# Kernel optimization log

Measured on AMD Instinct MI355X. Metric: run time of the kernel, lower is better.

Reference implementation:

```python
import math
import jax, jax.numpy as jnp
import numpy as np

B, S, H = 4, 2048, 1024      # batch, seq_len, hidden_size
E, K, I = 8, 2, 1024         # n_routed_experts, top_k, expert intermediate
NSH = 2                      # n_shared_experts -> shared intermediate = NSH*I
CF, RSF = 1.25, 1.0          # capacity_factor, routed_scaling_factor


def setup_inputs() -> dict:
    key = jax.random.key(0)
    ks = jax.random.split(key, 8)
    w = lambda k, sh: jax.random.normal(k, sh, dtype=jnp.float32) * 0.02
    return {
        "hidden_states": jax.random.normal(ks[0], (B, S, H), dtype=jnp.float32),
        "gate_w":  w(ks[1], (E, H)),          # router weight (torch Linear layout)
        "we_gate": w(ks[2], (E, I, H)),       # per-expert gate_proj
        "we_up":   w(ks[3], (E, I, H)),       # per-expert up_proj
        "we_down": w(ks[4], (E, H, I)),       # per-expert down_proj
        "ws_gate": w(ks[5], (NSH * I, H)),    # shared expert gate_proj
        "ws_up":   w(ks[6], (NSH * I, H)),
        "ws_down": w(ks[7], (H, NSH * I)),
    }


def reference(hidden_states, gate_w, we_gate, we_up, we_down, ws_gate, ws_up, ws_down):
    orig_shape = hidden_states.shape
    x = hidden_states.reshape(-1, H)                       # [N, H]
    N = x.shape[0]

    # ---- gate (fp32 softmax + top-k, normalized, scaled) ----
    logits = x.astype(jnp.float32) @ gate_w.astype(jnp.float32).T   # [N, E]
    scores = jax.nn.softmax(logits, axis=-1)
    topk_w, topk_idx = jax.lax.top_k(scores, K)                      # [N, K]
    topk_w = topk_w / (topk_w.sum(-1, keepdims=True) + 1e-20) * RSF  # norm_topk_prob

    # ---- capacity masking: position of each (token,k) slot within its expert ----
    capacity = math.ceil(CF * N * K / E)
    flat = topk_idx.reshape(-1)                                      # [N*K]
    one_hot = jax.nn.one_hot(flat, E, dtype=jnp.int32)               # [N*K, E]
    pos = jnp.cumsum(one_hot, axis=0) - 1                            # running count per expert
    pos_tok = jnp.take_along_axis(pos, flat[:, None], axis=1)[:, 0]  # [N*K]
    keep = (pos_tok < capacity).reshape(N, K)
    topk_w = topk_w * keep.astype(topk_w.dtype)

    # ---- combine weights per (token, expert); dropped slots contribute 0 ----
    comb = jnp.zeros((N, E), jnp.float32).at[jnp.arange(N)[:, None], topk_idx].add(topk_w)

    # ---- routed experts: dense SwiGLU per expert, weighted combine ----
    g = jnp.einsum('nh,eih->nei', x, we_gate)                        # [N, E, I]
    u = jnp.einsum('nh,eih->nei', x, we_up)
    eo = jnp.einsum('nei,ehi->neh', jax.nn.silu(g) * u, we_down)     # [N, E, H]
    y = jnp.einsum('neh,ne->nh', eo, comb)                           # [N, H]

    # ---- shared experts ----
    sh = (jax.nn.silu(x @ ws_gate.T) * (x @ ws_up.T)) @ ws_down.T    # [N, H]

    return (y + sh).reshape(orig_shape)
```

## Files before the change

kernel.cpp:

```cpp
#include <hip/hip_runtime.h>

typedef unsigned short u16;

#define NTOK 8192
#define HD   1024
#define NEXP 8
#define CAP  2560

typedef __bf16 bf16x8 __attribute__((ext_vector_type(8)));
typedef float  f32x4  __attribute__((ext_vector_type(4)));

__device__ __forceinline__ u16 f2bf(float f){
  union { float f; unsigned u; } v; v.f = f;
  return (u16)((v.u + 0x7fffu + ((v.u >> 16) & 1u)) >> 16);
}
__device__ __forceinline__ float bf2f(u16 h){
  union { unsigned u; float f; } v; v.u = ((unsigned)h) << 16; return v.f;
}

__device__ __forceinline__ void async16(const void* g, void* l){
  __builtin_amdgcn_global_load_lds((__attribute__((address_space(1))) void*)(g),
                                   (__attribute__((address_space(3))) void*)(l), 16, 0, 0);
}

__global__ __launch_bounds__(256)
void prep_kernel(const float* __restrict__ x, const float* __restrict__ gate_w,
                 const float* __restrict__ we_gate, const float* __restrict__ we_up,
                 const float* __restrict__ we_down, const float* __restrict__ ws_gate,
                 const float* __restrict__ ws_up, const float* __restrict__ ws_down,
                 u16* __restrict__ x_bf, u16* __restrict__ wg_bf, u16* __restrict__ wu_bf,
                 u16* __restrict__ wd_bf, u16* __restrict__ wsg_bf, u16* __restrict__ wsu_bf,
                 u16* __restrict__ wsd_bf,
                 int* __restrict__ topk_idx, float* __restrict__ topk_w){
  __shared__ float gw[NEXP * HD];
  int bid = blockIdx.x;
  int t = threadIdx.x;
  if (bid < 2048){
    for (int i = t; i < NEXP * HD; i += 256) gw[i] = gate_w[i];
    __syncthreads();
    int wave = t >> 6, l = t & 63;
    int tok = bid * 4 + wave;
    const float* xr = x + (size_t)tok * HD;
    double acc[NEXP];
#pragma unroll
    for (int e = 0; e < NEXP; e++) acc[e] = 0.0;
    for (int j = 0; j < 16; j++){
      int h = j * 64 + l;
      double xv = (double)xr[h];
#pragma unroll
      for (int e = 0; e < NEXP; e++) acc[e] += xv * (double)gw[e * HD + h];
    }
#pragma unroll
    for (int e = 0; e < NEXP; e++){
      double v = acc[e];
#pragma unroll
      for (int off = 32; off > 0; off >>= 1) v += __shfl_down(v, off, 64);
      acc[e] = v;
    }
    if (l == 0){
      int i0 = 0; double l0 = acc[0];
#pragma unroll
      for (int e = 1; e < NEXP; e++) if (acc[e] > l0){ l0 = acc[e]; i0 = e; }
      int i1 = -1; double l1 = -1e300;
#pragma unroll
      for (int e = 0; e < NEXP; e++) if (e != i0 && acc[e] > l1){ l1 = acc[e]; i1 = e; }
      double e1 = exp(l1 - l0);
      double s  = 1.0 + e1;
      topk_idx[tok * 2 + 0] = i0;
      topk_idx[tok * 2 + 1] = i1;
      topk_w [tok * 2 + 0] = (float)(1.0 / s);
      topk_w [tok * 2 + 1] = (float)(e1 / s);
    }
  } else {
    long long g = (long long)(bid - 2048) * 256 + t;
    const float4* s; ushort4* d; long long off;
    if      (g <  2097152){ s = (const float4*)x;       d = (ushort4*)x_bf;   off = 0; }
    else if (g <  4194304){ s = (const float4*)we_gate; d = (ushort4*)wg_bf;  off = 2097152; }
    else if (g <  6291456){ s = (const float4*)we_up;   d = (ushort4*)wu_bf;  off = 4194304; }
    else if (g <  8388608){ s = (const float4*)we_down; d = (ushort4*)wd_bf;  off = 6291456; }
    else if (g <  8912896){ s = (const float4*)ws_gate; d = (ushort4*)wsg_bf; off = 8388608; }
    else if (g <  9437184){ s = (const float4*)ws_up;   d = (ushort4*)wsu_bf; off = 8912896; }
    else                  { s = (const float4*)ws_down; d = (ushort4*)wsd_bf; off = 9437184; }
    long long i = g - off;
    float4 v = s[i];
    ushort4 o;
    o.x = f2bf(v.x); o.y = f2bf(v.y); o.z = f2bf(v.z); o.w = f2bf(v.w);
    d[i] = o;
  }
}

__global__ __launch_bounds__(256) void scan_kernel(const int* __restrict__ topk_idx,
                                                   const float* __restrict__ topk_w,
                                                   int* __restrict__ tok_list,
                                                   float* __restrict__ w_list,
                                                   int* __restrict__ slot_map,
                                                   int* __restrict__ ne){
  __shared__ int hist[256][NEXP];
  int t = threadIdx.x;
  const int SPT = (NTOK * 2) / 256;
  int cnt[NEXP];
#pragma unroll
  for (int e = 0; e < NEXP; e++) cnt[e] = 0;
  int base = t * SPT;
  for (int s = 0; s < SPT; s++) cnt[topk_idx[base + s]]++;
#pragma unroll
  for (int e = 0; e < NEXP; e++) hist[t][e] = cnt[e];
  __syncthreads();
  if (t < NEXP){
    int run = 0;
    for (int i = 0; i < 256; i++){ int v = hist[i][t]; hist[i][t] = run; run += v; }
    ne[t] = run < CAP ? run : CAP;
  }
  __syncthreads();
  int pos[NEXP];
#pragma unroll
  for (int e = 0; e < NEXP; e++) pos[e] = hist[t][e];
  for (int s = 0; s < SPT; s++){
    int slot = base + s;
    int e = topk_idx[slot];
    int p = pos[e]++;
    if (p < CAP){
      tok_list[e * CAP + p] = slot >> 1;
      w_list [e * CAP + p] = topk_w[slot];
      slot_map[slot] = e * CAP + p;
    } else {
      slot_map[slot] = -1;
    }
  }
}

__global__ __launch_bounds__(256)
void gu_kernel(const u16* __restrict__ x_bf,
               const u16* __restrict__ wg, const u16* __restrict__ wu,
               const u16* __restrict__ wsg, const u16* __restrict__ wsu,
               u16* __restrict__ Hr, u16* __restrict__ Hs,
               const int* __restrict__ tok_list, const int* __restrict__ ne)
{
  __shared__ u16 As[128 * 64];
  __shared__ u16 Bs[128 * 64];

  const int bid = blockIdx.x;
  const bool routed = bid < 2560;
  int m0, n0, ldc, n_valid;
  const u16 *B0, *B1;
  u16* C;
  const int* tl = nullptr;
  if (routed){
    int e = bid / 320, r = bid % 320;
    m0 = (r / 16) * 128; n0 = (r % 16) * 64;
    B0 = wg + (size_t)e * (1024 * 1024);
    B1 = wu + (size_t)e * (1024 * 1024);
    C  = Hr + (size_t)e * (CAP * 1024);
    ldc = 1024;
    n_valid = ne[e];
    tl = tok_list + e * CAP;
    if (m0 >= n_valid) return;
  } else {
    int b2 = bid - 2560;
    n0 = (b2 / 64) * 64; m0 = (b2 % 64) * 128;
    B0 = wsg; B1 = wsu; C = Hs; ldc = 2048; n_valid = 1 << 30;
  }

  const int tid = threadIdx.x;
  const int wv  = tid >> 6;
  const int l   = tid & 63;
  const int lr  = l >> 3;
  const int cb  = (l & 7) ^ lr;

  const u16* aptr[4];
  const u16* bptr[4];
#pragma unroll
  for (int i = 0; i < 4; i++){
    int chunk = i * 4 + wv;
    int arow  = m0 + chunk * 8 + lr;
    if (routed){
      int r2 = arow < n_valid ? arow : (n_valid - 1);
      aptr[i] = x_bf + (size_t)tl[r2] * 1024 + cb * 8;
    } else {
      aptr[i] = x_bf + (size_t)arow * 1024 + cb * 8;
    }
    int rn = chunk * 8 + lr;
    int w  = rn >> 6;
    int jq = (rn >> 4) & 3;
    int rl = rn & 15;
    int icol = n0 + w * 32 + (jq & 1) * 16 + rl;
    bptr[i] = ((jq < 2) ? B0 : B1) + (size_t)icol * 1024 + cb * 8;
  }

  const int wm = wv & 1, wn = wv >> 1;
  const int col = l & 15, quad = l >> 4;
  const int rr = col & 7, ch = col >> 3;

  f32x4 acc[4][4];
#pragma unroll
  for (int i = 0; i < 4; i++)
#pragma unroll
    for (int j = 0; j < 4; j++)
      acc[i][j] = (f32x4){0.f, 0.f, 0.f, 0.f};

  for (int k0 = 0; k0 < 1024; k0 += 64){
#pragma unroll
    for (int i = 0; i < 4; i++){
      int chunk = i * 4 + wv;
      async16(aptr[i] + k0, &As[chunk * 512 + l * 8]);
      async16(bptr[i] + k0, &Bs[chunk * 512 + l * 8]);
    }
    __syncthreads();
#pragma unroll
    for (int s = 0; s < 2; s++){
      const int so = (rr * 8 + ((quad + s * 4) ^ rr)) * 8;
      bf16x8 a[4], b[4];
#pragma unroll
      for (int i = 0; i < 4; i++) a[i] = *(const bf16x8*)&As[(wm * 8 + i * 2 + ch) * 512 + so];
#pragma unroll
      for (int j = 0; j < 4; j++) b[j] = *(const bf16x8*)&Bs[(wn * 8 + j * 2 + ch) * 512 + so];
#pragma unroll
      for (int i = 0; i < 4; i++)
#pragma unroll
        for (int j = 0; j < 4; j++)
          acc[i][j] = __builtin_amdgcn_mfma_f32_16x16x32_bf16(a[i], b[j], acc[i][j], 0, 0, 0);
    }
    __syncthreads();
  }

#pragma unroll
  for (int i = 0; i < 4; i++)
#pragma unroll
    for (int r = 0; r < 4; r++){
      int row = m0 + wm * 64 + i * 16 + quad * 4 + r;
#pragma unroll
      for (int j = 0; j < 2; j++){
        int cg = n0 + wn * 32 + j * 16 + col;
        float g = acc[i][j][r], u = acc[i][j + 2][r];
        float h = (g / (1.f + __expf(-g))) * u;
        C[(size_t)row * ldc + cg] = f2bf(h);
      }
    }
}

#define MODE_WBF   1
#define MODE_FINAL 2

template<int MODE>
__global__ __launch_bounds__(256)
void gemm_bt(const u16* __restrict__ A, long long sAe,
             const u16* __restrict__ B0, long long sBe,
             void* __restrict__ Cv, long long sCe, int ldc,
             const float* __restrict__ w_list, const int* __restrict__ ne,
             const u16* __restrict__ Ebuf, const int* __restrict__ slot_map,
             int M, int K)
{
  __shared__ u16 As[128 * 64];
  __shared__ u16 Bs[128 * 64];

  const int e  = blockIdx.z;
  const int m0 = blockIdx.y * 128;
  const int n0 = blockIdx.x * 128;

  int n_valid = (MODE == MODE_WBF) ? ne[e] : M;
  if (m0 >= n_valid) return;

  const u16* Ae = A + (size_t)e * sAe;

  const int tid = threadIdx.x;
  const int wv  = tid >> 6;
  const int l   = tid & 63;
  const int lr  = l >> 3;
  const int cb  = (l & 7) ^ lr;

  const u16* aptr[4];
  const u16* bptr[4];
#pragma unroll
  for (int i = 0; i < 4; i++){
    int chunk = i * 4 + wv;
    int arow  = m0 + chunk * 8 + lr;
    aptr[i] = Ae + (size_t)arow * K + cb * 8;
    int brow = n0 + chunk * 8 + lr;
    bptr[i] = B0 + (size_t)e * sBe + (size_t)brow * K + cb * 8;
  }

  const int wm = wv & 1, wn = wv >> 1;
  const int col = l & 15, quad = l >> 4;
  const int rr = col & 7, ch = col >> 3;

  f32x4 acc[4][4];
#pragma unroll
  for (int i = 0; i < 4; i++)
#pragma unroll
    for (int j = 0; j < 4; j++)
      acc[i][j] = (f32x4){0.f, 0.f, 0.f, 0.f};

  for (int k0 = 0; k0 < K; k0 += 64){
#pragma unroll
    for (int i = 0; i < 4; i++){
      int chunk = i * 4 + wv;
      async16(aptr[i] + k0, &As[chunk * 512 + l * 8]);
      async16(bptr[i] + k0, &Bs[chunk * 512 + l * 8]);
    }
    __syncthreads();
#pragma unroll
    for (int s = 0; s < 2; s++){
      const int so = (rr * 8 + ((quad + s * 4) ^ rr)) * 8;
      bf16x8 a[4], b[4];
#pragma unroll
      for (int i = 0; i < 4; i++) a[i] = *(const bf16x8*)&As[(wm * 8 + i * 2 + ch) * 512 + so];
#pragma unroll
      for (int j = 0; j < 4; j++) b[j] = *(const bf16x8*)&Bs[(wn * 8 + j * 2 + ch) * 512 + so];
#pragma unroll
      for (int i = 0; i < 4; i++)
#pragma unroll
        for (int j = 0; j < 4; j++)
          acc[i][j] = __builtin_amdgcn_mfma_f32_16x16x32_bf16(a[i], b[j], acc[i][j], 0, 0, 0);
    }
    __syncthreads();
  }

  if (MODE == MODE_WBF){
    u16* C = (u16*)Cv + (size_t)e * sCe;
    const float* wl = w_list + e * CAP;
#pragma unroll
    for (int i = 0; i < 4; i++)
#pragma unroll
      for (int r = 0; r < 4; r++){
        int row = m0 + wm * 64 + i * 16 + quad * 4 + r;
        if (row < n_valid){
          float wgt = wl[row];
#pragma unroll
          for (int j = 0; j < 4; j++){
            int cg = n0 + wn * 64 + j * 16 + col;
            C[(size_t)row * ldc + cg] = f2bf(wgt * acc[i][j][r]);
          }
        }
      }
  } else {
    float* C = (float*)Cv;
#pragma unroll
    for (int i = 0; i < 4; i++)
#pragma unroll
      for (int r = 0; r < 4; r++){
        int row = m0 + wm * 64 + i * 16 + quad * 4 + r;
        int s0 = slot_map[row * 2 + 0];
        int s1 = slot_map[row * 2 + 1];
#pragma unroll
        for (int j = 0; j < 4; j++){
          int cg = n0 + wn * 64 + j * 16 + col;
          float v = acc[i][j][r];
          if (s0 >= 0) v += bf2f(Ebuf[(size_t)s0 * HD + cg]);
          if (s1 >= 0) v += bf2f(Ebuf[(size_t)s1 * HD + cg]);
          C[(size_t)row * HD + cg] = v;
        }
      }
  }
}

extern "C" void kernel_launch(void* const* d_in, const int* in_sizes, int n_in,
                              void* d_out, int out_size, void* d_ws, size_t ws_size,
                              hipStream_t stream){
  const float* x       = (const float*)d_in[0];
  const float* gate_w  = (const float*)d_in[1];
  const float* we_gate = (const float*)d_in[2];
  const float* we_up   = (const float*)d_in[3];
  const float* we_down = (const float*)d_in[4];
  const float* ws_gate = (const float*)d_in[5];
  const float* ws_up   = (const float*)d_in[6];
  const float* ws_down = (const float*)d_in[7];
  float* out = (float*)d_out;

  char* p = (char*)d_ws;
  u16* x_bf   = (u16*)p; p += (size_t)NTOK * HD * 2;
  u16* wg_bf  = (u16*)p; p += (size_t)NEXP * 1024 * 1024 * 2;
  u16* wu_bf  = (u16*)p; p += (size_t)NEXP * 1024 * 1024 * 2;
  u16* wsg_bf = (u16*)p; p += (size_t)2048 * 1024 * 2;
  u16* wsu_bf = (u16*)p; p += (size_t)2048 * 1024 * 2;
  u16* wd_bf  = (u16*)p; p += (size_t)NEXP * 1024 * 1024 * 2;
  u16* wsd_bf = (u16*)p; p += (size_t)1024 * 2048 * 2;
  u16* Hr     = (u16*)p; p += (size_t)NEXP * CAP * 1024 * 2;
  u16* Hs     = (u16*)p; p += (size_t)NTOK * 2048 * 2;
  int*   topk_idx = (int*)p;   p += (size_t)NTOK * 2 * 4;
  float* topk_w   = (float*)p; p += (size_t)NTOK * 2 * 4;
  int*   tok_list = (int*)p;   p += (size_t)NEXP * CAP * 4;
  float* w_list   = (float*)p; p += (size_t)NEXP * CAP * 4;
  int*   slot_map = (int*)p;   p += (size_t)NTOK * 2 * 4;
  int*   ne       = (int*)p;   p += 128;
  u16* Ebuf = wg_bf;

  prep_kernel<<<dim3(40960), dim3(256), 0, stream>>>(
      x, gate_w, we_gate, we_up, we_down, ws_gate, ws_up, ws_down,
      x_bf, wg_bf, wu_bf, wd_bf, wsg_bf, wsu_bf, wsd_bf, topk_idx, topk_w);

  scan_kernel<<<dim3(1), dim3(256), 0, stream>>>(topk_idx, topk_w, tok_list, w_list, slot_map, ne);

  gu_kernel<<<dim3(4608), dim3(256), 0, stream>>>(
      x_bf, wg_bf, wu_bf, wsg_bf, wsu_bf, Hr, Hs, tok_list, ne);

  const long long WEXP = 1024LL * 1024;
  const long long SLOT = (long long)CAP * 1024;

  gemm_bt<MODE_WBF><<<dim3(8, 20, 8), 256, 0, stream>>>(
      Hr, SLOT, wd_bf, WEXP, Ebuf, SLOT, 1024,
      w_list, ne, nullptr, nullptr, CAP, 1024);

  gemm_bt<MODE_FINAL><<<dim3(8, 64, 1), 256, 0, stream>>>(
      Hs, 0, wsd_bf, 0, out, 0, 1024,
      w_list, ne, Ebuf, slot_map, NTOK, 2048);
}
```

Before: 555.7 us.

## Parallelize routing scan, merge down GEMMs into one launch, split combine

The single-block scan becomes a two-pass multi-block scan that uses wave ballots and popcounts to assign capacity positions. The routed and shared down-projection GEMMs now run in one launch, so their blocks can occupy the device together. The gather-add of routed outputs moves into a separate vectorized combine kernel. Expert block indexing is interleaved across experts in the gate-up kernel, which may spread weight traffic across blocks. The costs are one extra launch and an extra full read and write of the output for the combine.

```diff
diff --git a/kernel.cpp b/kernel.cpp
--- a/kernel.cpp
+++ b/kernel.cpp
@@ -89,43 +89,71 @@
   }
 }
 
-__global__ __launch_bounds__(256) void scan_kernel(const int* __restrict__ topk_idx,
-                                                   const float* __restrict__ topk_w,
-                                                   int* __restrict__ tok_list,
-                                                   float* __restrict__ w_list,
-                                                   int* __restrict__ slot_map,
-                                                   int* __restrict__ ne){
-  __shared__ int hist[256][NEXP];
-  int t = threadIdx.x;
-  const int SPT = (NTOK * 2) / 256;
-  int cnt[NEXP];
-#pragma unroll
-  for (int e = 0; e < NEXP; e++) cnt[e] = 0;
-  int base = t * SPT;
-  for (int s = 0; s < SPT; s++) cnt[topk_idx[base + s]]++;
-#pragma unroll
-  for (int e = 0; e < NEXP; e++) hist[t][e] = cnt[e];
+__global__ __launch_bounds__(256)
+void scan_p1(const int* __restrict__ topk_idx, int* __restrict__ chunk_hist){
+  __shared__ int wcnt[4 * NEXP];
+  int t = threadIdx.x, w = t >> 6, l = t & 63;
+  int my_e = topk_idx[blockIdx.x * 256 + t];
+#pragma unroll
+  for (int e = 0; e < NEXP; e++){
+    unsigned long long m = __ballot(my_e == e);
+    if (l == e) wcnt[w * NEXP + e] = __popcll(m);
+  }
+  __syncthreads();
+  if (t < NEXP){
+    int s = 0;
+#pragma unroll
+    for (int w2 = 0; w2 < 4; w2++) s += wcnt[w2 * NEXP + t];
+    chunk_hist[blockIdx.x * NEXP + t] = s;
+  }
+}
+
+__global__ __launch_bounds__(256)
+void scan_p2(const int* __restrict__ topk_idx, const float* __restrict__ topk_w,
+             const int* __restrict__ chunk_hist,
+             int* __restrict__ tok_list, float* __restrict__ w_list,
+             int* __restrict__ slot_map, int* __restrict__ ne){
+  __shared__ int hist_s[64 * NEXP];
+  __shared__ int base_s[NEXP];
+  __shared__ int wcnt[4 * NEXP];
+  int t = threadIdx.x, w = t >> 6, l = t & 63;
+  int chunk = blockIdx.x;
+#pragma unroll
+  for (int i = 0; i < 2; i++) hist_s[i * 256 + t] = chunk_hist[i * 256 + t];
+  __syncthreads();
+  if (t < NEXP){
+    int b = 0, tot = 0;
+    for (int c = 0; c < 64; c++){
+      if (c == chunk) b = tot;
+      tot += hist_s[c * NEXP + t];
+    }
+    base_s[t] = b;
+    if (chunk == 0) ne[t] = tot < CAP ? tot : CAP;
+  }
+  int slot = chunk * 256 + t;
+  int my_e = topk_idx[slot];
+  float my_w = topk_w[slot];
+  unsigned long long mymask = 0;
+#pragma unroll
+  for (int e = 0; e < NEXP; e++){
+    unsigned long long m = __ballot(my_e == e);
+    if (my_e == e) mymask = m;
+    if (l == e) wcnt[w * NEXP + e] = __popcll(m);
+  }
   __syncthreads();
   if (t < NEXP){
     int run = 0;
-    for (int i = 0; i < 256; i++){ int v = hist[i][t]; hist[i][t] = run; run += v; }
-    ne[t] = run < CAP ? run : CAP;
+#pragma unroll
+    for (int w2 = 0; w2 < 4; w2++){ int v = wcnt[w2 * NEXP + t]; wcnt[w2 * NEXP + t] = run; run += v; }
   }
   __syncthreads();
-  int pos[NEXP];
-#pragma unroll
-  for (int e = 0; e < NEXP; e++) pos[e] = hist[t][e];
-  for (int s = 0; s < SPT; s++){
-    int slot = base + s;
-    int e = topk_idx[slot];
-    int p = pos[e]++;
-    if (p < CAP){
-      tok_list[e * CAP + p] = slot >> 1;
-      w_list [e * CAP + p] = topk_w[slot];
-      slot_map[slot] = e * CAP + p;
-    } else {
-      slot_map[slot] = -1;
-    }
+  int pos = base_s[my_e] + wcnt[w * NEXP + my_e] + __popcll(mymask & ((1ull << l) - 1ull));
+  if (pos < CAP){
+    tok_list[my_e * CAP + pos] = slot >> 1;
+    w_list [my_e * CAP + pos] = my_w;
+    slot_map[slot] = my_e * CAP + pos;
+  } else {
+    slot_map[slot] = -1;
   }
 }
 
@@ -146,8 +174,8 @@
   u16* C;
   const int* tl = nullptr;
   if (routed){
-    int e = bid / 320, r = bid % 320;
-    m0 = (r / 16) * 128; n0 = (r % 16) * 64;
+    int e = bid & 7, r = bid >> 3;
+    m0 = (r >> 4) * 128; n0 = (r & 15) * 64;
     B0 = wg + (size_t)e * (1024 * 1024);
     B1 = wu + (size_t)e * (1024 * 1024);
     C  = Hr + (size_t)e * (CAP * 1024);
@@ -238,29 +266,32 @@
     }
 }
 
-#define MODE_WBF   1
-#define MODE_FINAL 2
-
-template<int MODE>
-__global__ __launch_bounds__(256)
-void gemm_bt(const u16* __restrict__ A, long long sAe,
-             const u16* __restrict__ B0, long long sBe,
-             void* __restrict__ Cv, long long sCe, int ldc,
-             const float* __restrict__ w_list, const int* __restrict__ ne,
-             const u16* __restrict__ Ebuf, const int* __restrict__ slot_map,
-             int M, int K)
+__global__ __launch_bounds__(256)
+void down_kernel(const u16* __restrict__ Hr, const u16* __restrict__ wd,
+                 const u16* __restrict__ Hs, const u16* __restrict__ wsd,
+                 u16* __restrict__ Ebuf, float* __restrict__ out,
+                 const float* __restrict__ w_list, const int* __restrict__ ne)
 {
   __shared__ u16 As[128 * 64];
   __shared__ u16 Bs[128 * 64];
 
-  const int e  = blockIdx.z;
-  const int m0 = blockIdx.y * 128;
-  const int n0 = blockIdx.x * 128;
-
-  int n_valid = (MODE == MODE_WBF) ? ne[e] : M;
-  if (m0 >= n_valid) return;
-
-  const u16* Ae = A + (size_t)e * sAe;
+  const int bid = blockIdx.x;
+  const bool routed = bid < 1280;
+  int m0, n0, n_valid, K, e = 0;
+  const u16 *Ab, *Bb;
+  if (routed){
+    e = bid & 7; int r = bid >> 3;
+    m0 = (r >> 3) * 128; n0 = (r & 7) * 128;
+    Ab = Hr + (size_t)e * (CAP * 1024);
+    Bb = wd + (size_t)e * (1024 * 1024);
+    K = 1024;
+    n_valid = ne[e];
+    if (m0 >= n_valid) return;
+  } else {
+    int b2 = bid - 1280;
+    n0 = (b2 & 7) * 128; m0 = (b2 >> 3) * 128;
+    Ab = Hs; Bb = wsd; K = 2048; n_valid = 1 << 30;
+  }
 
   const int tid = threadIdx.x;
   const int wv  = tid >> 6;
@@ -273,10 +304,8 @@
 #pragma unroll
   for (int i = 0; i < 4; i++){
     int chunk = i * 4 + wv;
-    int arow  = m0 + chunk * 8 + lr;
-    aptr[i] = Ae + (size_t)arow * K + cb * 8;
-    int brow = n0 + chunk * 8 + lr;
-    bptr[i] = B0 + (size_t)e * sBe + (size_t)brow * K + cb * 8;
+    aptr[i] = Ab + (size_t)(m0 + chunk * 8 + lr) * K + cb * 8;
+    bptr[i] = Bb + (size_t)(n0 + chunk * 8 + lr) * K + cb * 8;
   }
 
   const int wm = wv & 1, wn = wv >> 1;
@@ -315,8 +344,8 @@
     __syncthreads();
   }
 
-  if (MODE == MODE_WBF){
-    u16* C = (u16*)Cv + (size_t)e * sCe;
+  if (routed){
+    u16* C = Ebuf + (size_t)e * (CAP * 1024);
     const float* wl = w_list + e * CAP;
 #pragma unroll
     for (int i = 0; i < 4; i++)
@@ -328,29 +357,43 @@
 #pragma unroll
           for (int j = 0; j < 4; j++){
             int cg = n0 + wn * 64 + j * 16 + col;
-            C[(size_t)row * ldc + cg] = f2bf(wgt * acc[i][j][r]);
+            C[(size_t)row * 1024 + cg] = f2bf(wgt * acc[i][j][r]);
           }
         }
       }
   } else {
-    float* C = (float*)Cv;
 #pragma unroll
     for (int i = 0; i < 4; i++)
 #pragma unroll
       for (int r = 0; r < 4; r++){
         int row = m0 + wm * 64 + i * 16 + quad * 4 + r;
-        int s0 = slot_map[row * 2 + 0];
-        int s1 = slot_map[row * 2 + 1];
 #pragma unroll
         for (int j = 0; j < 4; j++){
           int cg = n0 + wn * 64 + j * 16 + col;
-          float v = acc[i][j][r];
-          if (s0 >= 0) v += bf2f(Ebuf[(size_t)s0 * HD + cg]);
-          if (s1 >= 0) v += bf2f(Ebuf[(size_t)s1 * HD + cg]);
-          C[(size_t)row * HD + cg] = v;
+          out[(size_t)row * 1024 + cg] = acc[i][j][r];
         }
       }
   }
+}
+
+__global__ __launch_bounds__(256)
+void combine_kernel(float* __restrict__ out, const u16* __restrict__ Ebuf,
+                    const int* __restrict__ slot_map){
+  long long g = (long long)blockIdx.x * 256 + threadIdx.x;
+  int row = (int)(g >> 8);
+  int c4  = (int)(g & 255);
+  int s0 = slot_map[row * 2 + 0];
+  int s1 = slot_map[row * 2 + 1];
+  float4 v = ((float4*)out)[g];
+  if (s0 >= 0){
+    ushort4 a = ((const ushort4*)Ebuf)[(size_t)s0 * 256 + c4];
+    v.x += bf2f(a.x); v.y += bf2f(a.y); v.z += bf2f(a.z); v.w += bf2f(a.w);
+  }
+  if (s1 >= 0){
+    ushort4 a = ((const ushort4*)Ebuf)[(size_t)s1 * 256 + c4];
+    v.x += bf2f(a.x); v.y += bf2f(a.y); v.z += bf2f(a.z); v.w += bf2f(a.w);
+  }
+  ((float4*)out)[g] = v;
 }
 
 extern "C" void kernel_launch(void* const* d_in, const int* in_sizes, int n_in,
@@ -376,31 +419,28 @@
   u16* wsd_bf = (u16*)p; p += (size_t)1024 * 2048 * 2;
   u16* Hr     = (u16*)p; p += (size_t)NEXP * CAP * 1024 * 2;
   u16* Hs     = (u16*)p; p += (size_t)NTOK * 2048 * 2;
-  int*   topk_idx = (int*)p;   p += (size_t)NTOK * 2 * 4;
-  float* topk_w   = (float*)p; p += (size_t)NTOK * 2 * 4;
-  int*   tok_list = (int*)p;   p += (size_t)NEXP * CAP * 4;
-  float* w_list   = (float*)p; p += (size_t)NEXP * CAP * 4;
-  int*   slot_map = (int*)p;   p += (size_t)NTOK * 2 * 4;
-  int*   ne       = (int*)p;   p += 128;
+  int*   topk_idx   = (int*)p;   p += (size_t)NTOK * 2 * 4;
+  float* topk_w     = (float*)p; p += (size_t)NTOK * 2 * 4;
+  int*   tok_list   = (int*)p;   p += (size_t)NEXP * CAP * 4;
+  float* w_list     = (float*)p; p += (size_t)NEXP * CAP * 4;
+  int*   slot_map   = (int*)p;   p += (size_t)NTOK * 2 * 4;
+  int*   chunk_hist = (int*)p;   p += 64 * NEXP * 4;
+  int*   ne         = (int*)p;   p += 128;
   u16* Ebuf = wg_bf;
 
   prep_kernel<<<dim3(40960), dim3(256), 0, stream>>>(
       x, gate_w, we_gate, we_up, we_down, ws_gate, ws_up, ws_down,
       x_bf, wg_bf, wu_bf, wd_bf, wsg_bf, wsu_bf, wsd_bf, topk_idx, topk_w);
 
-  scan_kernel<<<dim3(1), dim3(256), 0, stream>>>(topk_idx, topk_w, tok_list, w_list, slot_map, ne);
+  scan_p1<<<dim3(64), dim3(256), 0, stream>>>(topk_idx, chunk_hist);
+  scan_p2<<<dim3(64), dim3(256), 0, stream>>>(topk_idx, topk_w, chunk_hist,
+                                              tok_list, w_list, slot_map, ne);
 
   gu_kernel<<<dim3(4608), dim3(256), 0, stream>>>(
       x_bf, wg_bf, wu_bf, wsg_bf, wsu_bf, Hr, Hs, tok_list, ne);
 
-  const long long WEXP = 1024LL * 1024;
-  const long long SLOT = (long long)CAP * 1024;
-
-  gemm_bt<MODE_WBF><<<dim3(8, 20, 8), 256, 0, stream>>>(
-      Hr, SLOT, wd_bf, WEXP, Ebuf, SLOT, 1024,
-      w_list, ne, nullptr, nullptr, CAP, 1024);
-
-  gemm_bt<MODE_FINAL><<<dim3(8, 64, 1), 256, 0, stream>>>(
-      Hs, 0, wsd_bf, 0, out, 0, 1024,
-      w_list, ne, Ebuf, slot_map, NTOK, 2048);
-}
+  down_kernel<<<dim3(1792), dim3(256), 0, stream>>>(
+      Hr, wd_bf, Hs, wsd_bf, Ebuf, out, w_list, ne);
+
+  combine_kernel<<<dim3(8192), dim3(256), 0, stream>>>(out, Ebuf, slot_map);
+}
```

After: 486.5 us. -12.5%, faster.
